# Performance work log

Measured on AMD Instinct MI355X. Metric: run time of the kernel, lower is better.

The kernel has to match this reference:

```python
import jax, jax.numpy as jnp
import numpy as np

EMB = 1024
HEADS = 16
BLOCK = 128


def setup_inputs() -> dict:
    key = jax.random.key(0)
    k1, k2, k3 = jax.random.split(key, 3)
    B, T, C = 4, 4096, EMB
    x = jax.random.normal(k1, (B, T, C), dtype=jnp.float32)
    # Linear weights stored as [in, out] (i.e. torch W.T); qkv has no bias.
    W_qkv = jax.random.normal(k2, (C, 3 * C), dtype=jnp.float32) * 0.02
    W_proj = jax.random.normal(k3, (C, C), dtype=jnp.float32) * 0.02
    b_proj = jnp.zeros((C,), dtype=jnp.float32)
    return {"x": x, "W_qkv": W_qkv, "W_proj": W_proj, "b_proj": b_proj}


def reference(x, W_qkv, W_proj, b_proj):
    # Dropout is inference-mode identity.
    B, T, C = x.shape
    H, D, BS = HEADS, C // HEADS, BLOCK
    nb = T // BS  # number of local blocks
    qkv = x @ W_qkv  # [B,T,3C]
    q, k, v = jnp.split(qkv, 3, axis=-1)
    # [B, nb, BS, H, D] -- each block attends only within itself
    q = q.reshape(B, nb, BS, H, D)
    k = k.reshape(B, nb, BS, H, D)
    v = v.reshape(B, nb, BS, H, D)
    scores = jnp.einsum("bnqhd,bnkhd->bnhqk", q, k) / jnp.sqrt(jnp.float32(D))
    # is_decoder: causal tril within each diagonal block (tril[i:end, i:end])
    tril = jnp.tril(jnp.ones((BS, BS), dtype=bool))
    scores = jnp.where(tril, scores, -jnp.inf)
    # faithful to original: stable exp, then divide by (sum + 1e-6)
    scores = scores - jnp.max(scores, axis=-1, keepdims=True)
    e = jnp.exp(scores)
    p = e / (jnp.sum(e, axis=-1, keepdims=True) + 1e-6)
    out = jnp.einsum("bnhqk,bnkhd->bnqhd", p, v).reshape(B, T, C)
    return out @ W_proj + b_proj
```

## Files before the change

### kernel.cpp

```cpp
#include <hip/hip_runtime.h>
#include <hip/hip_bf16.h>
#include <math.h>


typedef __bf16 bf16_t;
typedef __bf16 bf16x8 __attribute__((ext_vector_type(8)));
typedef float  f32x4  __attribute__((ext_vector_type(4)));

typedef const __attribute__((address_space(1))) void* gptr_t;
typedef __attribute__((address_space(3))) void* lptr_t;

__global__ __launch_bounds__(256) void cvt_f32_bf16(const float* __restrict__ in,
                                                    bf16_t* __restrict__ out, size_t n) {
    size_t stride = (size_t)gridDim.x * blockDim.x * 4;
    for (size_t i = ((size_t)blockIdx.x * blockDim.x + threadIdx.x) * 4; i < n; i += stride) {
        float4 v = *(const float4*)(in + i);
        bf16_t t[4];
        t[0] = (bf16_t)v.x; t[1] = (bf16_t)v.y; t[2] = (bf16_t)v.z; t[3] = (bf16_t)v.w;
        *(uint2*)(out + i) = *(uint2*)t;
    }
}

__global__ __launch_bounds__(256) void transpose_cvt(const float* __restrict__ in,
                                                     bf16_t* __restrict__ out, int K, int N) {
    __shared__ float tile[32][33];
    const int tx = threadIdx.x & 31, ty = threadIdx.x >> 5;
    const int bx = blockIdx.x, by = blockIdx.y;
    #pragma unroll
    for (int i = 0; i < 4; i++) {
        const int k = by * 32 + ty + i * 8;
        tile[ty + i * 8][tx] = in[(size_t)k * N + bx * 32 + tx];
    }
    __syncthreads();
    #pragma unroll
    for (int i = 0; i < 4; i++) {
        const int n = bx * 32 + ty + i * 8;
        out[(size_t)n * K + by * 32 + tx] = (bf16_t)tile[tx][ty + i * 8];
    }
}

template <bool BF16_OUT, bool BIAS>
__global__ __launch_bounds__(512) void gemm128(const bf16_t* __restrict__ A,
                                               const bf16_t* __restrict__ Bt,
                                               void* __restrict__ Cout,
                                               const float* __restrict__ bias,
                                               int M, int N, int K) {
    __shared__ bf16_t ring[3][12288];

    const int tid  = threadIdx.x;
    const int lane = tid & 63, wave = tid >> 6;
    const int quad = lane >> 4, l16 = lane & 15;
    const int wm = wave >> 2, wn = wave & 3;

    const int nbm  = M >> 7;
    const int mloc = nbm >> 3;
    const int xcd  = blockIdx.x & 7;
    const int idx  = blockIdx.x >> 3;
    const int bn   = idx / mloc;
    const int bm   = xcd * mloc + (idx - bn * mloc);

    const bf16_t* Ab = A  + (size_t)bm * 128 * K;
    const bf16_t* Bb = Bt + (size_t)bn * 256 * K;

    const int srow = lane >> 2;
    const int scs  = (lane & 3) ^ ((srow >> 1) & 3);
    const int rdo  = ((quad ^ ((l16 >> 1) & 3)) << 3);

    f32x4 acc[4][4];
    #pragma unroll
    for (int i = 0; i < 4; ++i)
        #pragma unroll
        for (int j = 0; j < 4; ++j) acc[i][j] = (f32x4){0.f, 0.f, 0.f, 0.f};

#define STG(SLICE, SLOT)                                                              \
    do {                                                                              \
        __builtin_amdgcn_global_load_lds(                                             \
            (gptr_t)(Ab + (size_t)(wave * 16 + srow) * K + ((SLICE) << 5) + scs * 8), \
            (lptr_t)&ring[SLOT][wave * 512], 16, 0, 0);                               \
        __builtin_amdgcn_global_load_lds(                                             \
            (gptr_t)(Bb + (size_t)(wave * 32 + srow) * K + ((SLICE) << 5) + scs * 8), \
            (lptr_t)&ring[SLOT][4096 + wave * 1024], 16, 0, 0);                       \
        __builtin_amdgcn_global_load_lds(                                             \
            (gptr_t)(Bb + (size_t)(wave * 32 + 16 + srow) * K + ((SLICE) << 5) +      \
                     scs * 8),                                                        \
            (lptr_t)&ring[SLOT][4096 + wave * 1024 + 512], 16, 0, 0);                 \
    } while (0)

#define BODY(G, RS, SS, DO_STAGE, WAIT_STMT)                                          \
    do {                                                                              \
        const bf16_t* sl_ = ring[RS];                                                 \
        bf16x8 af_[4], bf_[4];                                                        \
        _Pragma("unroll")                                                             \
        for (int fr = 0; fr < 4; ++fr)                                                \
            af_[fr] = *(const bf16x8*)&sl_[(wm * 64 + fr * 16 + l16) * 32 + rdo];     \
        _Pragma("unroll")                                                             \
        for (int fr = 0; fr < 4; ++fr)                                                \
            bf_[fr] =                                                                 \
                *(const bf16x8*)&sl_[4096 + (wn * 64 + fr * 16 + l16) * 32 + rdo];    \
        if (DO_STAGE) STG((G) + 2, SS);                                               \
        asm volatile("s_waitcnt lgkmcnt(0)" ::: "memory");                            \
        WAIT_STMT;                                                                    \
        __builtin_amdgcn_s_barrier();                                                 \
        __builtin_amdgcn_s_setprio(1);                                                \
        _Pragma("unroll")                                                             \
        for (int mr = 0; mr < 4; ++mr)                                                \
            _Pragma("unroll")                                                         \
            for (int nr = 0; nr < 4; ++nr)                                            \
                acc[mr][nr] = __builtin_amdgcn_mfma_f32_16x16x32_bf16(                \
                    af_[mr], bf_[nr], acc[mr][nr], 0, 0, 0);                          \
        __builtin_amdgcn_s_setprio(0);                                                \
    } while (0)

    STG(0, 0); STG(1, 1);
    asm volatile("s_waitcnt vmcnt(3)" ::: "memory");
    __builtin_amdgcn_s_barrier();

    const int NS = K >> 5;
    int rs = 0, ss = 2;
    for (int g = 0; g < NS - 2; ++g) {
        BODY(g, rs, ss, true, asm volatile("s_waitcnt vmcnt(3)" ::: "memory"));
        rs = (rs == 2) ? 0 : rs + 1;
        ss = (ss == 2) ? 0 : ss + 1;
    }
    BODY(NS - 2, rs, ss, false, asm volatile("s_waitcnt vmcnt(0)" ::: "memory"));
    rs = (rs == 2) ? 0 : rs + 1;
    BODY(NS - 1, rs, ss, false, (void)0);
#undef BODY
#undef STG

    #pragma unroll
    for (int mr = 0; mr < 4; ++mr) {
        #pragma unroll
        for (int nr = 0; nr < 4; ++nr) {
            const int gcol = bn * 256 + wn * 64 + nr * 16 + l16;
            #pragma unroll
            for (int reg = 0; reg < 4; ++reg) {
                const int grow = bm * 128 + wm * 64 + mr * 16 + quad * 4 + reg;
                float v = acc[mr][nr][reg];
                if (BIAS) v += bias[gcol];
                if (BF16_OUT)
                    ((bf16_t*)Cout)[(size_t)grow * N + gcol] = (bf16_t)v;
                else
                    ((float*)Cout)[(size_t)grow * N + gcol] = v;
            }
        }
    }
}

__global__ __launch_bounds__(256, 3) void attn_kernel(const bf16_t* __restrict__ qkv,
                                                      bf16_t* __restrict__ attn_out) {
    __shared__ __align__(16) char smem[54272];
    bf16_t* qs = (bf16_t*)smem;
    bf16_t* ks = (bf16_t*)(smem + 18432);
    bf16_t* vT = (bf16_t*)(smem + 36864);
    bf16_t* ps = (bf16_t*)smem;

    const int tid = threadIdx.x;
    const int lane = tid & 63, wave = tid >> 6;
    const int quad = lane >> 4, l16 = lane & 15;

    const int bid = blockIdx.x;
    const int h = bid & 15;
    const int blk = (bid >> 4) & 31;
    const int b = bid >> 9;
    const int row0 = (b * 32 + blk) * 128;
    const int LDQ = 3072;

    for (int t = tid; t < 128 * 8; t += 256) {
        const int r = t >> 3;
        const int c = (t & 7) * 8;
        const bf16_t* src = qkv + (size_t)(row0 + r) * LDQ + h * 64;
        *(uint4*)&qs[r * 72 + c] = *(const uint4*)(src + c);
        *(uint4*)&ks[r * 72 + c] = *(const uint4*)(src + 1024 + c);
        bf16x8 vv = *(const bf16x8*)(src + 2048 + c);
        #pragma unroll
        for (int j = 0; j < 8; j++)
            vT[(c + j) * 136 + r] = vv[j];
    }
    __syncthreads();

    f32x4 sfrag[2][8];
    for (int mr = 0; mr < 2; mr++)
        for (int nc = 0; nc < 8; nc++)
            sfrag[mr][nc] = (f32x4){0.f, 0.f, 0.f, 0.f};

    #pragma unroll
    for (int ksl = 0; ksl < 2; ksl++) {
        bf16x8 aq[2], bk[8];
        #pragma unroll
        for (int mr = 0; mr < 2; mr++)
            aq[mr] = *(const bf16x8*)&qs[(wave * 32 + mr * 16 + l16) * 72 + ksl * 32 + quad * 8];
        #pragma unroll
        for (int nc = 0; nc < 8; nc++)
            bk[nc] = *(const bf16x8*)&ks[(nc * 16 + l16) * 72 + ksl * 32 + quad * 8];
        #pragma unroll
        for (int mr = 0; mr < 2; mr++)
            #pragma unroll
            for (int nc = 0; nc < 8; nc++)
                sfrag[mr][nc] = __builtin_amdgcn_mfma_f32_16x16x32_bf16(aq[mr], bk[nc], sfrag[mr][nc], 0, 0, 0);
    }

    #pragma unroll
    for (int mr = 0; mr < 2; mr++) {
        #pragma unroll
        for (int nc = 0; nc < 8; nc++) {
            #pragma unroll
            for (int reg = 0; reg < 4; reg++) {
                const int row = wave * 32 + mr * 16 + quad * 4 + reg;
                const int col = nc * 16 + l16;
                float s = sfrag[mr][nc][reg] * 0.125f;
                if (col > row) s = -INFINITY;
                sfrag[mr][nc][reg] = s;
            }
        }
    }

    #pragma unroll
    for (int mr = 0; mr < 2; mr++) {
        #pragma unroll
        for (int reg = 0; reg < 4; reg++) {
            float m = -INFINITY;
            #pragma unroll
            for (int nc = 0; nc < 8; nc++) m = fmaxf(m, sfrag[mr][nc][reg]);
            #pragma unroll
            for (int off = 1; off < 16; off <<= 1) m = fmaxf(m, __shfl_xor(m, off));
            float sum = 0.f;
            #pragma unroll
            for (int nc = 0; nc < 8; nc++) {
                float e = __expf(sfrag[mr][nc][reg] - m);
                sfrag[mr][nc][reg] = e;
                sum += e;
            }
            #pragma unroll
            for (int off = 1; off < 16; off <<= 1) sum += __shfl_xor(sum, off);
            const float inv = 1.0f / (sum + 1e-6f);
            #pragma unroll
            for (int nc = 0; nc < 8; nc++) sfrag[mr][nc][reg] *= inv;
        }
    }

    __syncthreads();

    #pragma unroll
    for (int mr = 0; mr < 2; mr++)
        #pragma unroll
        for (int nc = 0; nc < 8; nc++)
            #pragma unroll
            for (int reg = 0; reg < 4; reg++) {
                const int row = wave * 32 + mr * 16 + quad * 4 + reg;
                const int col = nc * 16 + l16;
                ps[row * 136 + col] = (bf16_t)sfrag[mr][nc][reg];
            }
    __syncthreads();

    f32x4 oacc[2][4];
    for (int mr = 0; mr < 2; mr++)
        for (int nd = 0; nd < 4; nd++)
            oacc[mr][nd] = (f32x4){0.f, 0.f, 0.f, 0.f};

    #pragma unroll
    for (int ksl = 0; ksl < 4; ksl++) {
        bf16x8 ap[2];
        #pragma unroll
        for (int mr = 0; mr < 2; mr++)
            ap[mr] = *(const bf16x8*)&ps[(wave * 32 + mr * 16 + l16) * 136 + ksl * 32 + quad * 8];
        #pragma unroll
        for (int nd = 0; nd < 4; nd++) {
            bf16x8 bv = *(const bf16x8*)&vT[(nd * 16 + l16) * 136 + ksl * 32 + quad * 8];
            #pragma unroll
            for (int mr = 0; mr < 2; mr++)
                oacc[mr][nd] = __builtin_amdgcn_mfma_f32_16x16x32_bf16(ap[mr], bv, oacc[mr][nd], 0, 0, 0);
        }
    }

    #pragma unroll
    for (int mr = 0; mr < 2; mr++)
        #pragma unroll
        for (int nd = 0; nd < 4; nd++)
            #pragma unroll
            for (int reg = 0; reg < 4; reg++) {
                const int row = row0 + wave * 32 + mr * 16 + quad * 4 + reg;
                const int col = h * 64 + nd * 16 + l16;
                attn_out[(size_t)row * 1024 + col] = (bf16_t)oacc[mr][nd][reg];
            }
}

extern "C" void kernel_launch(void* const* d_in, const int* in_sizes, int n_in,
                              void* d_out, int out_size, void* d_ws, size_t ws_size,
                              hipStream_t stream) {
    const float* x     = (const float*)d_in[0];
    const float* Wqkv  = (const float*)d_in[1];
    const float* Wproj = (const float*)d_in[2];
    const float* bproj = (const float*)d_in[3];

    const int M = 16384, C = 1024, N1 = 3072;

    char* ws = (char*)d_ws;
    bf16_t* xb     = (bf16_t*)(ws);
    bf16_t* wqkvT  = (bf16_t*)(ws + 33554432);
    bf16_t* wprojT = (bf16_t*)(ws + 39845888);
    bf16_t* qkvb   = (bf16_t*)(ws + 41943040);
    bf16_t* attnb  = (bf16_t*)(ws + 142606336);

    cvt_f32_bf16<<<8192, 256, 0, stream>>>(x, xb, (size_t)M * C);
    transpose_cvt<<<dim3(N1 / 32, C / 32), 256, 0, stream>>>(Wqkv, wqkvT, C, N1);
    transpose_cvt<<<dim3(C / 32, C / 32), 256, 0, stream>>>(Wproj, wprojT, C, C);

    gemm128<true, false><<<(N1 / 256) * (M / 128), 512, 0, stream>>>(
        xb, wqkvT, (void*)qkvb, nullptr, M, N1, C);

    attn_kernel<<<2048, 256, 0, stream>>>(qkvb, attnb);

    gemm128<false, true><<<(C / 256) * (M / 128), 512, 0, stream>>>(
        attnb, wprojT, d_out, bproj, M, C, C);
}
```

Before: 325.7 us.

## Retile GEMMs to 256x128 with four waves each, fuse prepass conversion kernels

The GEMM kernel now uses a 256x128 block tile with four waves. Each wave computes a 128x64 sub-tile holding 8x4 MFMA accumulators, where before eight waves each computed 64x64 of a 128x256 tile. This raises MFMA work per LDS fragment load and allows two blocks per CU, at the cost of more accumulator registers per wave. The three preprocessing kernels (x conversion and two weight transposes) are also merged into one launch to save launch overhead.

```diff
diff --git a/kernel.cpp b/kernel.cpp
--- a/kernel.cpp
+++ b/kernel.cpp
@@ -10,22 +10,38 @@
 typedef const __attribute__((address_space(1))) void* gptr_t;
 typedef __attribute__((address_space(3))) void* lptr_t;
 
-__global__ __launch_bounds__(256) void cvt_f32_bf16(const float* __restrict__ in,
-                                                    bf16_t* __restrict__ out, size_t n) {
-    size_t stride = (size_t)gridDim.x * blockDim.x * 4;
-    for (size_t i = ((size_t)blockIdx.x * blockDim.x + threadIdx.x) * 4; i < n; i += stride) {
-        float4 v = *(const float4*)(in + i);
-        bf16_t t[4];
-        t[0] = (bf16_t)v.x; t[1] = (bf16_t)v.y; t[2] = (bf16_t)v.z; t[3] = (bf16_t)v.w;
-        *(uint2*)(out + i) = *(uint2*)t;
-    }
-}
-
-__global__ __launch_bounds__(256) void transpose_cvt(const float* __restrict__ in,
-                                                     bf16_t* __restrict__ out, int K, int N) {
+__global__ __launch_bounds__(256) void prepass(const float* __restrict__ x,
+                                               bf16_t* __restrict__ xb,
+                                               const float* __restrict__ Wqkv,
+                                               bf16_t* __restrict__ wqkvT,
+                                               const float* __restrict__ Wproj,
+                                               bf16_t* __restrict__ wprojT) {
     __shared__ float tile[32][33];
+    const int bid = blockIdx.x;
+    if (bid < 8192) {
+        const size_t n = (size_t)16384 * 1024;
+        const size_t stride = (size_t)8192 * 256 * 4;
+        for (size_t i = ((size_t)bid * 256 + threadIdx.x) * 4; i < n; i += stride) {
+            float4 v = *(const float4*)(x + i);
+            bf16_t t[4];
+            t[0] = (bf16_t)v.x; t[1] = (bf16_t)v.y; t[2] = (bf16_t)v.z; t[3] = (bf16_t)v.w;
+            *(uint2*)(xb + i) = *(uint2*)t;
+        }
+        return;
+    }
+    const float* in;
+    bf16_t* out;
+    int K, N, bx, by;
+    if (bid < 8192 + 3072) {
+        const int t = bid - 8192;
+        in = Wqkv; out = wqkvT; K = 1024; N = 3072;
+        bx = t % 96; by = t / 96;
+    } else {
+        const int t = bid - 11264;
+        in = Wproj; out = wprojT; K = 1024; N = 1024;
+        bx = t & 31; by = t >> 5;
+    }
     const int tx = threadIdx.x & 31, ty = threadIdx.x >> 5;
-    const int bx = blockIdx.x, by = blockIdx.y;
     #pragma unroll
     for (int i = 0; i < 4; i++) {
         const int k = by * 32 + ty + i * 8;
@@ -40,70 +56,72 @@
 }
 
 template <bool BF16_OUT, bool BIAS>
-__global__ __launch_bounds__(512) void gemm128(const bf16_t* __restrict__ A,
-                                               const bf16_t* __restrict__ Bt,
-                                               void* __restrict__ Cout,
-                                               const float* __restrict__ bias,
-                                               int M, int N, int K) {
+__global__ __launch_bounds__(256, 2) void gemm256x128(const bf16_t* __restrict__ A,
+                                                      const bf16_t* __restrict__ Bt,
+                                                      void* __restrict__ Cout,
+                                                      const float* __restrict__ bias,
+                                                      int M, int N, int K) {
     __shared__ bf16_t ring[3][12288];
 
     const int tid  = threadIdx.x;
     const int lane = tid & 63, wave = tid >> 6;
     const int quad = lane >> 4, l16 = lane & 15;
-    const int wm = wave >> 2, wn = wave & 3;
-
-    const int nbm  = M >> 7;
+    const int wm = wave >> 1, wn = wave & 1;
+
+    const int nbm  = M >> 8;
     const int mloc = nbm >> 3;
     const int xcd  = blockIdx.x & 7;
     const int idx  = blockIdx.x >> 3;
     const int bn   = idx / mloc;
     const int bm   = xcd * mloc + (idx - bn * mloc);
 
-    const bf16_t* Ab = A  + (size_t)bm * 128 * K;
-    const bf16_t* Bb = Bt + (size_t)bn * 256 * K;
+    const bf16_t* Ab = A  + (size_t)bm * 256 * K;
+    const bf16_t* Bb = Bt + (size_t)bn * 128 * K;
 
     const int srow = lane >> 2;
     const int scs  = (lane & 3) ^ ((srow >> 1) & 3);
     const int rdo  = ((quad ^ ((l16 >> 1) & 3)) << 3);
 
-    f32x4 acc[4][4];
-    #pragma unroll
-    for (int i = 0; i < 4; ++i)
+    f32x4 acc[8][4];
+    #pragma unroll
+    for (int i = 0; i < 8; ++i)
         #pragma unroll
         for (int j = 0; j < 4; ++j) acc[i][j] = (f32x4){0.f, 0.f, 0.f, 0.f};
 
 #define STG(SLICE, SLOT)                                                              \
     do {                                                                              \
-        __builtin_amdgcn_global_load_lds(                                             \
-            (gptr_t)(Ab + (size_t)(wave * 16 + srow) * K + ((SLICE) << 5) + scs * 8), \
-            (lptr_t)&ring[SLOT][wave * 512], 16, 0, 0);                               \
-        __builtin_amdgcn_global_load_lds(                                             \
-            (gptr_t)(Bb + (size_t)(wave * 32 + srow) * K + ((SLICE) << 5) + scs * 8), \
-            (lptr_t)&ring[SLOT][4096 + wave * 1024], 16, 0, 0);                       \
-        __builtin_amdgcn_global_load_lds(                                             \
-            (gptr_t)(Bb + (size_t)(wave * 32 + 16 + srow) * K + ((SLICE) << 5) +      \
-                     scs * 8),                                                        \
-            (lptr_t)&ring[SLOT][4096 + wave * 1024 + 512], 16, 0, 0);                 \
+        _Pragma("unroll")                                                             \
+        for (int i_ = 0; i_ < 4; ++i_)                                                \
+            __builtin_amdgcn_global_load_lds(                                         \
+                (gptr_t)(Ab + (size_t)(wave * 64 + i_ * 16 + srow) * K +              \
+                         ((SLICE) << 5) + scs * 8),                                   \
+                (lptr_t)&ring[SLOT][(wave * 64 + i_ * 16) * 32], 16, 0, 0);           \
+        _Pragma("unroll")                                                             \
+        for (int i_ = 0; i_ < 2; ++i_)                                                \
+            __builtin_amdgcn_global_load_lds(                                         \
+                (gptr_t)(Bb + (size_t)(wave * 32 + i_ * 16 + srow) * K +              \
+                         ((SLICE) << 5) + scs * 8),                                   \
+                (lptr_t)&ring[SLOT][8192 + (wave * 32 + i_ * 16) * 32], 16, 0, 0);    \
     } while (0)
 
 #define BODY(G, RS, SS, DO_STAGE, WAIT_STMT)                                          \
     do {                                                                              \
         const bf16_t* sl_ = ring[RS];                                                 \
-        bf16x8 af_[4], bf_[4];                                                        \
-        _Pragma("unroll")                                                             \
-        for (int fr = 0; fr < 4; ++fr)                                                \
-            af_[fr] = *(const bf16x8*)&sl_[(wm * 64 + fr * 16 + l16) * 32 + rdo];     \
+        bf16x8 af_[8], bf_[4];                                                        \
+        _Pragma("unroll")                                                             \
+        for (int fr = 0; fr < 8; ++fr)                                                \
+            af_[fr] = *(const bf16x8*)&sl_[(wm * 128 + fr * 16 + l16) * 32 + rdo];    \
         _Pragma("unroll")                                                             \
         for (int fr = 0; fr < 4; ++fr)                                                \
             bf_[fr] =                                                                 \
-                *(const bf16x8*)&sl_[4096 + (wn * 64 + fr * 16 + l16) * 32 + rdo];    \
+                *(const bf16x8*)&sl_[8192 + (wn * 64 + fr * 16 + l16) * 32 + rdo];    \
         if (DO_STAGE) STG((G) + 2, SS);                                               \
         asm volatile("s_waitcnt lgkmcnt(0)" ::: "memory");                            \
         WAIT_STMT;                                                                    \
         __builtin_amdgcn_s_barrier();                                                 \
         __builtin_amdgcn_s_setprio(1);                                                \
         _Pragma("unroll")                                                             \
-        for (int mr = 0; mr < 4; ++mr)                                                \
+        for (int mr = 0; mr < 8; ++mr)                                                \
             _Pragma("unroll")                                                         \
             for (int nr = 0; nr < 4; ++nr)                                            \
                 acc[mr][nr] = __builtin_amdgcn_mfma_f32_16x16x32_bf16(                \
@@ -112,13 +130,13 @@
     } while (0)
 
     STG(0, 0); STG(1, 1);
-    asm volatile("s_waitcnt vmcnt(3)" ::: "memory");
+    asm volatile("s_waitcnt vmcnt(6)" ::: "memory");
     __builtin_amdgcn_s_barrier();
 
     const int NS = K >> 5;
     int rs = 0, ss = 2;
     for (int g = 0; g < NS - 2; ++g) {
-        BODY(g, rs, ss, true, asm volatile("s_waitcnt vmcnt(3)" ::: "memory"));
+        BODY(g, rs, ss, true, asm volatile("s_waitcnt vmcnt(6)" ::: "memory"));
         rs = (rs == 2) ? 0 : rs + 1;
         ss = (ss == 2) ? 0 : ss + 1;
     }
@@ -129,13 +147,13 @@
 #undef STG
 
     #pragma unroll
-    for (int mr = 0; mr < 4; ++mr) {
+    for (int mr = 0; mr < 8; ++mr) {
         #pragma unroll
         for (int nr = 0; nr < 4; ++nr) {
-            const int gcol = bn * 256 + wn * 64 + nr * 16 + l16;
+            const int gcol = bn * 128 + wn * 64 + nr * 16 + l16;
             #pragma unroll
             for (int reg = 0; reg < 4; ++reg) {
-                const int grow = bm * 128 + wm * 64 + mr * 16 + quad * 4 + reg;
+                const int grow = bm * 256 + wm * 128 + mr * 16 + quad * 4 + reg;
                 float v = acc[mr][nr][reg];
                 if (BIAS) v += bias[gcol];
                 if (BF16_OUT)
@@ -302,15 +320,13 @@
     bf16_t* qkvb   = (bf16_t*)(ws + 41943040);
     bf16_t* attnb  = (bf16_t*)(ws + 142606336);
 
-    cvt_f32_bf16<<<8192, 256, 0, stream>>>(x, xb, (size_t)M * C);
-    transpose_cvt<<<dim3(N1 / 32, C / 32), 256, 0, stream>>>(Wqkv, wqkvT, C, N1);
-    transpose_cvt<<<dim3(C / 32, C / 32), 256, 0, stream>>>(Wproj, wprojT, C, C);
-
-    gemm128<true, false><<<(N1 / 256) * (M / 128), 512, 0, stream>>>(
+    prepass<<<12288, 256, 0, stream>>>(x, xb, Wqkv, wqkvT, Wproj, wprojT);
+
+    gemm256x128<true, false><<<(N1 / 128) * (M / 256), 256, 0, stream>>>(
         xb, wqkvT, (void*)qkvb, nullptr, M, N1, C);
 
     attn_kernel<<<2048, 256, 0, stream>>>(qkvb, attnb);
 
-    gemm128<false, true><<<(C / 256) * (M / 128), 512, 0, stream>>>(
+    gemm256x128<false, true><<<(C / 128) * (M / 256), 256, 0, stream>>>(
         attnb, wprojT, d_out, bproj, M, C, C);
 }
```

New measurement: 315.2 us. 3.2% less time.
